# Optimization experiments

Measured on AMD Instinct MI355X. Metric: run time of the kernel, lower is better.

The kernel has to match this reference:

```python
import jax, jax.numpy as jnp
import numpy as np

B, S, H, V, NL = 64, 2048, 512, 50257, 2

def setup_inputs() -> dict:
    key = jax.random.key(0)
    ks = jax.random.split(key, 20)
    s = 0.02
    return {
        "input_ids": jax.random.randint(ks[0], (B,), 0, V),
        "hidden": jax.random.normal(ks[1], (NL, B, H), jnp.float32),
        "block_attn_weights": jax.random.uniform(ks[2], (B, 32), jnp.float32),
        "encoder_outputs": jax.random.normal(ks[3], (B, S, H), jnp.float32),
        "n_blocks": 32,
        "emb": jax.random.normal(ks[4], (V, H), jnp.float32) * s,
        "attn_W": jax.random.normal(ks[5], (H, H), jnp.float32) * s,
        "attn_b": jnp.zeros((H,), jnp.float32),
        "W_ih0": jax.random.normal(ks[6], (3 * H, 2 * H), jnp.float32) * s,
        "W_hh0": jax.random.normal(ks[7], (3 * H, H), jnp.float32) * s,
        "b_ih0": jnp.zeros((3 * H,), jnp.float32),
        "b_hh0": jnp.zeros((3 * H,), jnp.float32),
        "W_ih1": jax.random.normal(ks[8], (3 * H, H), jnp.float32) * s,
        "W_hh1": jax.random.normal(ks[9], (3 * H, H), jnp.float32) * s,
        "b_ih1": jnp.zeros((3 * H,), jnp.float32),
        "b_hh1": jnp.zeros((3 * H,), jnp.float32),
        "out_W": jax.random.normal(ks[10], (V, 2 * H), jnp.float32) * s,
        "out_b": jnp.zeros((V,), jnp.float32),
    }

def _gru_cell(x, h, W_ih, W_hh, b_ih, b_hh):
    gx = x @ W_ih.T + b_ih            # [B, 3H]
    gh = h @ W_hh.T + b_hh            # [B, 3H]
    xr, xz, xn = jnp.split(gx, 3, axis=-1)
    hr, hz, hn = jnp.split(gh, 3, axis=-1)
    r = jax.nn.sigmoid(xr + hr)
    z = jax.nn.sigmoid(xz + hz)
    n = jnp.tanh(xn + r * hn)
    return (1.0 - z) * n + z * h

def reference(input_ids, hidden, block_attn_weights, encoder_outputs, n_blocks,
              emb, attn_W, attn_b, W_ih0, W_hh0, b_ih0, b_hh0,
              W_ih1, W_hh1, b_ih1, b_hh1, out_W, out_b):
    b, s, h = encoder_outputs.shape
    L = s // n_blocks
    eo = encoder_outputs.reshape(b, n_blocks, L, h)          # [B,N,L,H]
    # Luong general score: h_dec . (W e + b), per block
    energy = jnp.einsum('bnlh,gh->bnlg', eo, attn_W) + attn_b  # [B,N,L,H]
    scores = jnp.einsum('bh,bnlh->bnl', hidden[-1], energy)    # [B,N,L]
    attn_w = jax.nn.softmax(scores, axis=-1)                   # [B,N,L]
    block_ctx = jnp.einsum('bnl,bnlh->bnh', attn_w, eo)        # [B,N,H]
    context = jnp.einsum('bn,bnh->bh', block_attn_weights, block_ctx)  # [B,H]
    embedded = emb[input_ids]                                  # [B,H]
    x = jnp.concatenate([embedded, context], axis=-1)          # [B,2H]
    h0 = _gru_cell(x, hidden[0], W_ih0, W_hh0, b_ih0, b_hh0)
    h1 = _gru_cell(h0, hidden[1], W_ih1, W_hh1, b_ih1, b_hh1)
    new_hidden = jnp.stack([h0, h1], axis=0)                   # [NL,B,H]
    out_in = jnp.concatenate([h1, context], axis=-1)           # [B,2H]
    log_probs = jax.nn.log_softmax(out_in @ out_W.T + out_b, axis=-1)  # [B,V]
    return (log_probs, new_hidden, context, attn_w)
```

## Files before the change

### kernel.cpp

```cpp
#include <hip/hip_runtime.h>

#define B_  64
#define S_  2048
#define H_  512
#define V_  50257
#define NB_ 32
#define L_  64
#define H3_ 1536

typedef float  f32x4  __attribute__((ext_vector_type(4)));
typedef __bf16 bf16x8 __attribute__((ext_vector_type(8)));

struct alignas(16) U4 { unsigned int x, y, z, w; };

__device__ __forceinline__ unsigned int f2bf_bits(float f) {
  unsigned int u = __float_as_uint(f);
  return (u + 0x7fffu + ((u >> 16) & 1u)) >> 16;
}

__device__ __forceinline__ float wave_sum(float v) {
#pragma unroll
  for (int off = 32; off > 0; off >>= 1) v += __shfl_xor(v, off, 64);
  return v;
}

__global__ __launch_bounds__(256) void k_q(const float* __restrict__ hidden,
                                           const float* __restrict__ attn_W,
                                           float* __restrict__ q) {
  __shared__ float sh[8 * H_];
  int tid = threadIdx.x;
  int h  = blockIdx.x * 256 + tid;
  int b0 = blockIdx.y * 8;
  const float* h1 = hidden + B_ * H_;
  for (int i = tid; i < 8 * H_; i += 256) sh[i] = h1[b0 * H_ + i];
  __syncthreads();
  float acc[8] = {0.f, 0.f, 0.f, 0.f, 0.f, 0.f, 0.f, 0.f};
  for (int g = 0; g < H_; ++g) {
    float w = attn_W[(size_t)g * H_ + h];
#pragma unroll
    for (int bb = 0; bb < 8; ++bb) acc[bb] += sh[bb * H_ + g] * w;
  }
#pragma unroll
  for (int bb = 0; bb < 8; ++bb) q[(b0 + bb) * H_ + h] = acc[bb];
}

__global__ __launch_bounds__(256) void k_attn(
    const float* __restrict__ eo, const float* __restrict__ hidden,
    const float* __restrict__ attn_b, const float* __restrict__ q,
    float* __restrict__ bc, float* __restrict__ attnw_out) {
  int lane = threadIdx.x & 63;
  int idx  = blockIdx.x * 4 + (threadIdx.x >> 6);
  int b = idx >> 5, n = idx & 31;

  const float4* qv = (const float4*)(q + (size_t)b * H_);
  float4 q0 = qv[lane], q1 = qv[64 + lane];

  const float4* hv = (const float4*)(hidden + (size_t)B_ * H_ + (size_t)b * H_);
  const float4* av = (const float4*)attn_b;
  float4 hx = hv[lane], hy = hv[64 + lane];
  float4 ax = av[lane], ay = av[64 + lane];
  float c0 = hx.x*ax.x + hx.y*ax.y + hx.z*ax.z + hx.w*ax.w
           + hy.x*ay.x + hy.y*ay.y + hy.z*ay.z + hy.w*ay.w;
  c0 = wave_sum(c0);

  const float4* ev = (const float4*)(eo + (size_t)(b * NB_ + n) * L_ * H_);
  float m = -1e30f, s = 0.f, myscore = 0.f;
  float4 A0 = {0,0,0,0}, A1 = {0,0,0,0};
  for (int l = 0; l < L_; ++l) {
    float4 e0 = ev[l * 128 + lane];
    float4 e1 = ev[l * 128 + 64 + lane];
    float p = e0.x*q0.x + e0.y*q0.y + e0.z*q0.z + e0.w*q0.w
            + e1.x*q1.x + e1.y*q1.y + e1.z*q1.z + e1.w*q1.w;
    p = wave_sum(p) + c0;
    if (lane == l) myscore = p;
    float mnew  = fmaxf(m, p);
    float alpha = __expf(m - mnew);
    float w     = __expf(p - mnew);
    s = s * alpha + w;
    A0.x = A0.x*alpha + w*e0.x; A0.y = A0.y*alpha + w*e0.y;
    A0.z = A0.z*alpha + w*e0.z; A0.w = A0.w*alpha + w*e0.w;
    A1.x = A1.x*alpha + w*e1.x; A1.y = A1.y*alpha + w*e1.y;
    A1.z = A1.z*alpha + w*e1.z; A1.w = A1.w*alpha + w*e1.w;
    m = mnew;
  }
  float inv = 1.f / s;
  float4* bv = (float4*)(bc + (size_t)(b * NB_ + n) * H_);
  float4 o0 = {A0.x*inv, A0.y*inv, A0.z*inv, A0.w*inv};
  float4 o1 = {A1.x*inv, A1.y*inv, A1.z*inv, A1.w*inv};
  bv[lane] = o0; bv[64 + lane] = o1;
  attnw_out[(size_t)(b * NB_ + n) * L_ + lane] = __expf(myscore - m) * inv;
}

__global__ __launch_bounds__(512) void k_prep(
    const int* __restrict__ ids, const float* __restrict__ hidden,
    const float* __restrict__ baw, const float* __restrict__ emb,
    const float* __restrict__ bc, float* __restrict__ ctx,
    unsigned short* __restrict__ xcatb, unsigned short* __restrict__ h0b,
    unsigned short* __restrict__ h1b, float* __restrict__ out_ctx) {
  int b = blockIdx.x, h = threadIdx.x;
  int id = ids[b];
  float ev = emb[(size_t)id * H_ + h];
  float acc = 0.f;
  for (int n = 0; n < NB_; ++n)
    acc += baw[b * NB_ + n] * bc[(size_t)(b * NB_ + n) * H_ + h];
  ctx[b * H_ + h]      = acc;
  out_ctx[b * H_ + h]  = acc;
  xcatb[b * 1024 + h]        = (unsigned short)f2bf_bits(ev);
  xcatb[b * 1024 + 512 + h]  = (unsigned short)f2bf_bits(acc);
  h0b[b * H_ + h] = (unsigned short)f2bf_bits(hidden[b * H_ + h]);
  h1b[b * H_ + h] = (unsigned short)f2bf_bits(hidden[B_ * H_ + b * H_ + h]);
}

template <int JT>
__global__ __launch_bounds__(256) void k_mv64(
    const float* __restrict__ W, const float* __restrict__ bias,
    const unsigned short* __restrict__ A, float* __restrict__ C,
    int N, int K, int ldC) {
  int tid = threadIdx.x;
  int wv = tid >> 6, lane = tid & 63;
  int mrow = lane & 15, qd = lane >> 4;
  int jbase = blockIdx.x * (16 * JT);
  const unsigned short* ap = A + (size_t)(wv * 16 + mrow) * K + qd * 8;
  f32x4 acc[JT];
  size_t wo[JT];
#pragma unroll
  for (int t = 0; t < JT; ++t) {
    acc[t] = (f32x4){0.f, 0.f, 0.f, 0.f};
    int jr = jbase + t * 16 + mrow; if (jr > N - 1) jr = N - 1;
    wo[t] = (size_t)jr * K + qd * 8;
  }
  for (int k0 = 0; k0 < K; k0 += 32) {
    bf16x8 af = __builtin_bit_cast(bf16x8, *(const U4*)(ap + k0));
#pragma unroll
    for (int t = 0; t < JT; ++t) {
      const float* wp = W + wo[t] + k0;
      float4 w0 = *(const float4*)wp;
      float4 w1 = *(const float4*)(wp + 4);
      U4 braw;
      braw.x = f2bf_bits(w0.x) | (f2bf_bits(w0.y) << 16);
      braw.y = f2bf_bits(w0.z) | (f2bf_bits(w0.w) << 16);
      braw.z = f2bf_bits(w1.x) | (f2bf_bits(w1.y) << 16);
      braw.w = f2bf_bits(w1.z) | (f2bf_bits(w1.w) << 16);
      bf16x8 bf = __builtin_bit_cast(bf16x8, braw);
      acc[t] = __builtin_amdgcn_mfma_f32_16x16x32_bf16(af, bf, acc[t], 0, 0, 0);
    }
  }
#pragma unroll
  for (int t = 0; t < JT; ++t) {
    int j = jbase + t * 16 + mrow;
    if (j < N) {
      float bv = bias[j];
#pragma unroll
      for (int r = 0; r < 4; ++r) {
        int brow = wv * 16 + qd * 4 + r;
        C[(size_t)brow * ldC + j] = acc[t][r] + bv;
      }
    }
  }
}

__global__ __launch_bounds__(512) void k_gru(
    const float* __restrict__ gx, const float* __restrict__ gh,
    const float* __restrict__ hprev, float* __restrict__ hnew_out,
    unsigned short* __restrict__ hnew_bf, const float* __restrict__ ctx,
    unsigned short* __restrict__ outin) {
  int b = blockIdx.x, i = threadIdx.x;
  size_t g0 = (size_t)b * H3_ + i;
  float xr = gx[g0], xz = gx[g0 + 512], xn = gx[g0 + 1024];
  float hr = gh[g0], hz = gh[g0 + 512], hn = gh[g0 + 1024];
  float r  = 1.f / (1.f + __expf(-(xr + hr)));
  float z  = 1.f / (1.f + __expf(-(xz + hz)));
  float nn = tanhf(xn + r * hn);
  float hp = hprev[b * H_ + i];
  float h  = (1.f - z) * nn + z * hp;
  hnew_out[b * H_ + i] = h;
  hnew_bf[b * H_ + i]  = (unsigned short)f2bf_bits(h);
  if (outin) {
    outin[b * 1024 + i]       = (unsigned short)f2bf_bits(h);
    outin[b * 1024 + 512 + i] = (unsigned short)f2bf_bits(ctx[b * H_ + i]);
  }
}

__global__ __launch_bounds__(1024) void k_lsm(const float* __restrict__ logits,
                                              float* __restrict__ out) {
  int b = blockIdx.x, tid = threadIdx.x;
  int lane = tid & 63, wid = tid >> 6;
  const float* row = logits + (size_t)b * V_;
  __shared__ float red[16];
  float mx = -1e30f;
  for (int j = tid; j < V_; j += 1024) mx = fmaxf(mx, row[j]);
#pragma unroll
  for (int off = 32; off > 0; off >>= 1) mx = fmaxf(mx, __shfl_xor(mx, off, 64));
  if (lane == 0) red[wid] = mx;
  __syncthreads();
  if (tid == 0) {
    float v = red[0];
    for (int i = 1; i < 16; ++i) v = fmaxf(v, red[i]);
    red[0] = v;
  }
  __syncthreads();
  mx = red[0];
  __syncthreads();
  float s = 0.f;
  for (int j = tid; j < V_; j += 1024) s += __expf(row[j] - mx);
  s = wave_sum(s);
  if (lane == 0) red[wid] = s;
  __syncthreads();
  if (tid == 0) {
    float v = 0.f;
    for (int i = 0; i < 16; ++i) v += red[i];
    red[0] = logf(v);
  }
  __syncthreads();
  float lse = mx + red[0];
  for (int j = tid; j < V_; j += 1024) out[(size_t)b * V_ + j] = row[j] - lse;
}

extern "C" void kernel_launch(void* const* d_in, const int* in_sizes, int n_in,
                              void* d_out, int out_size, void* d_ws, size_t ws_size,
                              hipStream_t stream) {
  const int*   ids    = (const int*)d_in[0];
  const float* hidden = (const float*)d_in[1];
  const float* baw    = (const float*)d_in[2];
  const float* eo     = (const float*)d_in[3];
  const float* emb    = (const float*)d_in[5];
  const float* attn_W = (const float*)d_in[6];
  const float* attn_b = (const float*)d_in[7];
  const float* W_ih0  = (const float*)d_in[8];
  const float* W_hh0  = (const float*)d_in[9];
  const float* b_ih0  = (const float*)d_in[10];
  const float* b_hh0  = (const float*)d_in[11];
  const float* W_ih1  = (const float*)d_in[12];
  const float* W_hh1  = (const float*)d_in[13];
  const float* b_ih1  = (const float*)d_in[14];
  const float* b_hh1  = (const float*)d_in[15];
  const float* out_W  = (const float*)d_in[16];
  const float* out_b  = (const float*)d_in[17];
  float* out = (float*)d_out;

  char* ws = (char*)d_ws;
  float*          q      = (float*)(ws + 0);
  float*          bc     = (float*)(ws + 131072);
  float*          ctx    = (float*)(ws + 4325376);
  unsigned short* xcatb  = (unsigned short*)(ws + 4456448);
  unsigned short* h0b    = (unsigned short*)(ws + 4587520);
  unsigned short* h1b    = (unsigned short*)(ws + 4653056);
  unsigned short* h0nb   = (unsigned short*)(ws + 4718592);
  unsigned short* outinb = (unsigned short*)(ws + 4784128);
  float*          gx     = (float*)(ws + 4915200);
  float*          gh     = (float*)(ws + 5308416);
  float*          logits = (float*)(ws + 5701632);

  float* out_lp   = out;
  float* out_nh   = out + 3216448;
  float* out_ctx  = out + 3281984;
  float* out_attw = out + 3314752;

  k_q   <<<dim3(2, 8), 256, 0, stream>>>(hidden, attn_W, q);
  k_attn<<<512, 256, 0, stream>>>(eo, hidden, attn_b, q, bc, out_attw);
  k_prep<<<64, 512, 0, stream>>>(ids, hidden, baw, emb, bc, ctx, xcatb, h0b, h1b, out_ctx);

  k_mv64<1><<<96, 256, 0, stream>>>(W_ih0, b_ih0, xcatb, gx, H3_, 1024, H3_);
  k_mv64<1><<<96, 256, 0, stream>>>(W_hh0, b_hh0, h0b,   gh, H3_, 512,  H3_);
  k_gru<<<64, 512, 0, stream>>>(gx, gh, hidden, out_nh, h0nb,
                                (const float*)nullptr, (unsigned short*)nullptr);

  k_mv64<1><<<96, 256, 0, stream>>>(W_ih1, b_ih1, h0nb, gx, H3_, 512, H3_);
  k_mv64<1><<<96, 256, 0, stream>>>(W_hh1, b_hh1, h1b,  gh, H3_, 512, H3_);
  k_gru<<<64, 512, 0, stream>>>(gx, gh, hidden + B_ * H_, out_nh + B_ * H_, h0nb,
                                ctx, outinb);

  k_mv64<4><<<786, 256, 0, stream>>>(out_W, out_b, outinb, logits, V_, 1024, V_);
  k_lsm<<<64, 1024, 0, stream>>>(logits, out_lp);
}
```

Baseline: 774.6 us.

## Split attention blocks across waves, fuse GRU gate GEMMs, restructure output projection

The attention kernel now gives each block-row to a whole workgroup: four waves each handle 16 positions with an online softmax, then merge the partial max, sum and accumulators through shared memory. This raises the grid to 2048 workgroups for more parallelism. The input and hidden GEMV pairs for each GRU layer are merged into one launch, which removes launch overhead. The output projection is restructured so each weight row is loaded and converted to bf16 once and reused across all four batch tiles, instead of each wave reloading the weights. The q kernel uses smaller tiles to spread across more blocks.

```diff
diff --git a/kernel.cpp b/kernel.cpp
--- a/kernel.cpp
+++ b/kernel.cpp
@@ -24,32 +24,35 @@
   return v;
 }
 
-__global__ __launch_bounds__(256) void k_q(const float* __restrict__ hidden,
+__global__ __launch_bounds__(128) void k_q(const float* __restrict__ hidden,
                                            const float* __restrict__ attn_W,
                                            float* __restrict__ q) {
-  __shared__ float sh[8 * H_];
+  __shared__ float sh[4 * H_];
   int tid = threadIdx.x;
-  int h  = blockIdx.x * 256 + tid;
-  int b0 = blockIdx.y * 8;
+  int h  = blockIdx.x * 128 + tid;
+  int b0 = blockIdx.y * 4;
   const float* h1 = hidden + B_ * H_;
-  for (int i = tid; i < 8 * H_; i += 256) sh[i] = h1[b0 * H_ + i];
-  __syncthreads();
-  float acc[8] = {0.f, 0.f, 0.f, 0.f, 0.f, 0.f, 0.f, 0.f};
+  for (int i = tid; i < 4 * H_; i += 128) sh[i] = h1[b0 * H_ + i];
+  __syncthreads();
+  float acc[4] = {0.f, 0.f, 0.f, 0.f};
   for (int g = 0; g < H_; ++g) {
     float w = attn_W[(size_t)g * H_ + h];
 #pragma unroll
-    for (int bb = 0; bb < 8; ++bb) acc[bb] += sh[bb * H_ + g] * w;
-  }
-#pragma unroll
-  for (int bb = 0; bb < 8; ++bb) q[(b0 + bb) * H_ + h] = acc[bb];
+    for (int bb = 0; bb < 4; ++bb) acc[bb] += sh[bb * H_ + g] * w;
+  }
+#pragma unroll
+  for (int bb = 0; bb < 4; ++bb) q[(b0 + bb) * H_ + h] = acc[bb];
 }
 
 __global__ __launch_bounds__(256) void k_attn(
     const float* __restrict__ eo, const float* __restrict__ hidden,
     const float* __restrict__ attn_b, const float* __restrict__ q,
     float* __restrict__ bc, float* __restrict__ attnw_out) {
-  int lane = threadIdx.x & 63;
-  int idx  = blockIdx.x * 4 + (threadIdx.x >> 6);
+  __shared__ float sm[4], ss[4];
+  __shared__ float shA[4][H_];
+  int tid = threadIdx.x;
+  int wv = tid >> 6, lane = tid & 63;
+  int idx = blockIdx.x;
   int b = idx >> 5, n = idx & 31;
 
   const float4* qv = (const float4*)(q + (size_t)b * H_);
@@ -66,13 +69,14 @@
   const float4* ev = (const float4*)(eo + (size_t)(b * NB_ + n) * L_ * H_);
   float m = -1e30f, s = 0.f, myscore = 0.f;
   float4 A0 = {0,0,0,0}, A1 = {0,0,0,0};
-  for (int l = 0; l < L_; ++l) {
+  for (int lr = 0; lr < 16; ++lr) {
+    int l = wv * 16 + lr;
     float4 e0 = ev[l * 128 + lane];
     float4 e1 = ev[l * 128 + 64 + lane];
     float p = e0.x*q0.x + e0.y*q0.y + e0.z*q0.z + e0.w*q0.w
             + e1.x*q1.x + e1.y*q1.y + e1.z*q1.z + e1.w*q1.w;
     p = wave_sum(p) + c0;
-    if (lane == l) myscore = p;
+    if (lane == lr) myscore = p;
     float mnew  = fmaxf(m, p);
     float alpha = __expf(m - mnew);
     float w     = __expf(p - mnew);
@@ -83,12 +87,29 @@
     A1.z = A1.z*alpha + w*e1.z; A1.w = A1.w*alpha + w*e1.w;
     m = mnew;
   }
-  float inv = 1.f / s;
-  float4* bv = (float4*)(bc + (size_t)(b * NB_ + n) * H_);
-  float4 o0 = {A0.x*inv, A0.y*inv, A0.z*inv, A0.w*inv};
-  float4 o1 = {A1.x*inv, A1.y*inv, A1.z*inv, A1.w*inv};
-  bv[lane] = o0; bv[64 + lane] = o1;
-  attnw_out[(size_t)(b * NB_ + n) * L_ + lane] = __expf(myscore - m) * inv;
+  if (lane == 0) { sm[wv] = m; ss[wv] = s; }
+  __syncthreads();
+  float m_g = fmaxf(fmaxf(sm[0], sm[1]), fmaxf(sm[2], sm[3]));
+  float s_g = ss[0]*__expf(sm[0]-m_g) + ss[1]*__expf(sm[1]-m_g)
+            + ss[2]*__expf(sm[2]-m_g) + ss[3]*__expf(sm[3]-m_g);
+  float scale = __expf(m - m_g);
+  float4* pa = (float4*)&shA[wv][0];
+  float4 w0 = {A0.x*scale, A0.y*scale, A0.z*scale, A0.w*scale};
+  float4 w1 = {A1.x*scale, A1.y*scale, A1.z*scale, A1.w*scale};
+  pa[lane] = w0; pa[64 + lane] = w1;
+  __syncthreads();
+  float inv = 1.f / s_g;
+  float2 sum = {0.f, 0.f};
+#pragma unroll
+  for (int w = 0; w < 4; ++w) {
+    float2 v = ((float2*)&shA[w][0])[tid];
+    sum.x += v.x; sum.y += v.y;
+  }
+  float2* bv = (float2*)(bc + (size_t)(b * NB_ + n) * H_);
+  bv[tid] = (float2){sum.x * inv, sum.y * inv};
+  if (lane < 16)
+    attnw_out[(size_t)(b * NB_ + n) * L_ + wv * 16 + lane] =
+        __expf(myscore - m_g) * inv;
 }
 
 __global__ __launch_bounds__(512) void k_prep(
@@ -111,49 +132,82 @@
   h1b[b * H_ + h] = (unsigned short)f2bf_bits(hidden[B_ * H_ + b * H_ + h]);
 }
 
-template <int JT>
-__global__ __launch_bounds__(256) void k_mv64(
-    const float* __restrict__ W, const float* __restrict__ bias,
-    const unsigned short* __restrict__ A, float* __restrict__ C,
-    int N, int K, int ldC) {
+__global__ __launch_bounds__(256) void k_mv2(
+    const float* __restrict__ W1, const float* __restrict__ bias1,
+    const unsigned short* __restrict__ A1, float* __restrict__ C1, int K1,
+    const float* __restrict__ W2, const float* __restrict__ bias2,
+    const unsigned short* __restrict__ A2, float* __restrict__ C2, int K2) {
+  bool sec = blockIdx.x >= 96;
+  const float* W = sec ? W2 : W1;
+  const float* bias = sec ? bias2 : bias1;
+  const unsigned short* A = sec ? A2 : A1;
+  float* C = sec ? C2 : C1;
+  int K = sec ? K2 : K1;
+  int blk = sec ? blockIdx.x - 96 : blockIdx.x;
+
   int tid = threadIdx.x;
   int wv = tid >> 6, lane = tid & 63;
   int mrow = lane & 15, qd = lane >> 4;
-  int jbase = blockIdx.x * (16 * JT);
+  int j = blk * 16 + mrow;
   const unsigned short* ap = A + (size_t)(wv * 16 + mrow) * K + qd * 8;
-  f32x4 acc[JT];
-  size_t wo[JT];
-#pragma unroll
-  for (int t = 0; t < JT; ++t) {
-    acc[t] = (f32x4){0.f, 0.f, 0.f, 0.f};
-    int jr = jbase + t * 16 + mrow; if (jr > N - 1) jr = N - 1;
-    wo[t] = (size_t)jr * K + qd * 8;
-  }
+  const float* wp = W + (size_t)j * K + qd * 8;
+  f32x4 acc = (f32x4){0.f, 0.f, 0.f, 0.f};
   for (int k0 = 0; k0 < K; k0 += 32) {
     bf16x8 af = __builtin_bit_cast(bf16x8, *(const U4*)(ap + k0));
-#pragma unroll
-    for (int t = 0; t < JT; ++t) {
-      const float* wp = W + wo[t] + k0;
-      float4 w0 = *(const float4*)wp;
-      float4 w1 = *(const float4*)(wp + 4);
-      U4 braw;
-      braw.x = f2bf_bits(w0.x) | (f2bf_bits(w0.y) << 16);
-      braw.y = f2bf_bits(w0.z) | (f2bf_bits(w0.w) << 16);
-      braw.z = f2bf_bits(w1.x) | (f2bf_bits(w1.y) << 16);
-      braw.w = f2bf_bits(w1.z) | (f2bf_bits(w1.w) << 16);
-      bf16x8 bf = __builtin_bit_cast(bf16x8, braw);
-      acc[t] = __builtin_amdgcn_mfma_f32_16x16x32_bf16(af, bf, acc[t], 0, 0, 0);
+    float4 w0 = *(const float4*)(wp + k0);
+    float4 w1 = *(const float4*)(wp + k0 + 4);
+    U4 braw;
+    braw.x = f2bf_bits(w0.x) | (f2bf_bits(w0.y) << 16);
+    braw.y = f2bf_bits(w0.z) | (f2bf_bits(w0.w) << 16);
+    braw.z = f2bf_bits(w1.x) | (f2bf_bits(w1.y) << 16);
+    braw.w = f2bf_bits(w1.z) | (f2bf_bits(w1.w) << 16);
+    bf16x8 bf = __builtin_bit_cast(bf16x8, braw);
+    acc = __builtin_amdgcn_mfma_f32_16x16x32_bf16(af, bf, acc, 0, 0, 0);
+  }
+  float bv = bias[j];
+#pragma unroll
+  for (int r = 0; r < 4; ++r) {
+    int brow = wv * 16 + qd * 4 + r;
+    C[(size_t)brow * H3_ + j] = acc[r] + bv;
+  }
+}
+
+__global__ __launch_bounds__(256) void k_out(
+    const float* __restrict__ W, const float* __restrict__ bias,
+    const unsigned short* __restrict__ A, float* __restrict__ C) {
+  int tid = threadIdx.x;
+  int wv = tid >> 6, lane = tid & 63;
+  int mrow = lane & 15, qd = lane >> 4;
+  int j = blockIdx.x * 64 + wv * 16 + mrow;
+  int jc = j < V_ ? j : V_ - 1;
+  const float* wp = W + (size_t)jc * 1024 + qd * 8;
+  const unsigned short* ap = A + mrow * 1024 + qd * 8;
+  f32x4 acc[4];
+#pragma unroll
+  for (int r = 0; r < 4; ++r) acc[r] = (f32x4){0.f, 0.f, 0.f, 0.f};
+  for (int k0 = 0; k0 < 1024; k0 += 32) {
+    float4 w0 = *(const float4*)(wp + k0);
+    float4 w1 = *(const float4*)(wp + k0 + 4);
+    U4 braw;
+    braw.x = f2bf_bits(w0.x) | (f2bf_bits(w0.y) << 16);
+    braw.y = f2bf_bits(w0.z) | (f2bf_bits(w0.w) << 16);
+    braw.z = f2bf_bits(w1.x) | (f2bf_bits(w1.y) << 16);
+    braw.w = f2bf_bits(w1.z) | (f2bf_bits(w1.w) << 16);
+    bf16x8 bw = __builtin_bit_cast(bf16x8, braw);
+#pragma unroll
+    for (int r = 0; r < 4; ++r) {
+      bf16x8 af = __builtin_bit_cast(bf16x8, *(const U4*)(ap + r * 16 * 1024 + k0));
+      acc[r] = __builtin_amdgcn_mfma_f32_16x16x32_bf16(af, bw, acc[r], 0, 0, 0);
     }
   }
-#pragma unroll
-  for (int t = 0; t < JT; ++t) {
-    int j = jbase + t * 16 + mrow;
-    if (j < N) {
-      float bv = bias[j];
-#pragma unroll
-      for (int r = 0; r < 4; ++r) {
-        int brow = wv * 16 + qd * 4 + r;
-        C[(size_t)brow * ldC + j] = acc[t][r] + bv;
+  if (j < V_) {
+    float bv = bias[j];
+#pragma unroll
+    for (int r = 0; r < 4; ++r) {
+#pragma unroll
+      for (int g = 0; g < 4; ++g) {
+        int brow = r * 16 + qd * 4 + g;
+        C[(size_t)brow * V_ + j] = acc[r][g] + bv;
       }
     }
   }
@@ -256,20 +310,20 @@
   float* out_ctx  = out + 3281984;
   float* out_attw = out + 3314752;
 
-  k_q   <<<dim3(2, 8), 256, 0, stream>>>(hidden, attn_W, q);
-  k_attn<<<512, 256, 0, stream>>>(eo, hidden, attn_b, q, bc, out_attw);
+  k_q   <<<dim3(4, 16), 128, 0, stream>>>(hidden, attn_W, q);
+  k_attn<<<2048, 256, 0, stream>>>(eo, hidden, attn_b, q, bc, out_attw);
   k_prep<<<64, 512, 0, stream>>>(ids, hidden, baw, emb, bc, ctx, xcatb, h0b, h1b, out_ctx);
 
-  k_mv64<1><<<96, 256, 0, stream>>>(W_ih0, b_ih0, xcatb, gx, H3_, 1024, H3_);
-  k_mv64<1><<<96, 256, 0, stream>>>(W_hh0, b_hh0, h0b,   gh, H3_, 512,  H3_);
+  k_mv2<<<192, 256, 0, stream>>>(W_ih0, b_ih0, xcatb, gx, 1024,
+                                 W_hh0, b_hh0, h0b,   gh, 512);
   k_gru<<<64, 512, 0, stream>>>(gx, gh, hidden, out_nh, h0nb,
                                 (const float*)nullptr, (unsigned short*)nullptr);
 
-  k_mv64<1><<<96, 256, 0, stream>>>(W_ih1, b_ih1, h0nb, gx, H3_, 512, H3_);
-  k_mv64<1><<<96, 256, 0, stream>>>(W_hh1, b_hh1, h1b,  gh, H3_, 512, H3_);
+  k_mv2<<<192, 256, 0, stream>>>(W_ih1, b_ih1, h0nb, gx, 512,
+                                 W_hh1, b_hh1, h1b,  gh, 512);
   k_gru<<<64, 512, 0, stream>>>(gx, gh, hidden + B_ * H_, out_nh + B_ * H_, h0nb,
                                 ctx, outinb);
 
-  k_mv64<4><<<786, 256, 0, stream>>>(out_W, out_b, outinb, logits, V_, 1024, V_);
+  k_out<<<786, 256, 0, stream>>>(out_W, out_b, outinb, logits);
   k_lsm<<<64, 1024, 0, stream>>>(logits, out_lp);
 }
```

Result: faster. 701.3 us (-9.5%).
